# Optimization experiments

Hardware: AMD Instinct MI355X
Metric: run time of the kernel (lower is better)

## Reference

```python
import jax, jax.numpy as jnp
import numpy as np

ENT_N = 100000  # entity vocab (relation rows live inside this table, as in the source)
REL_N = 237
DIM = 128
N = 16384       # batch of triples
EPS = 1e-12     # F.normalize default eps


def _l2norm(x, axis=-1):
    n = jnp.linalg.norm(x, axis=axis, keepdims=True)
    return x / jnp.maximum(n, EPS)


def setup_inputs() -> dict:
    key = jax.random.key(0)
    k1, k2, k3, k4 = jax.random.split(key, 4)
    ent_emb = jax.random.normal(k1, (ENT_N, DIM), dtype=jnp.float32)
    h_ids = jax.random.randint(k2, (N,), 0, ENT_N)
    r_typ = jax.random.randint(k3, (N,), 0, REL_N)
    t_ids = jax.random.randint(k4, (N,), 0, ENT_N)
    return {"ent_emb": ent_emb, "h_ids": h_ids, "r_typ": r_typ, "t_ids": t_ids}


def reference(ent_emb, h_ids, r_typ, t_ids):
    d = ent_emb.shape[1]
    h = _l2norm(ent_emb[h_ids])           # [n, d]
    t = _l2norm(ent_emb[t_ids])           # [n, d]
    # The torch loop looks up ent_emb[r_typ*d + k] for k in range(d); gather
    # the whole relation block at once instead of d tiny lookups + cat.
    r_idx = r_typ[:, None] * d + jnp.arange(d)  # [n, d]
    R = ent_emb[r_idx]                     # [n, d, d]; row k = relation vec k
    prod = jnp.einsum('nd,nkd->nk', h, R)  # [n, d]
    prod = _l2norm(prod)
    return jnp.linalg.norm(prod - t, axis=1)  # [n]
```

## Files before the change

kernel.cpp:

```cpp
#include <hip/hip_runtime.h>

#define RELS 237
#define DIM 128
#define CH 32
#define MAXCHUNK 742
#define PREPB 64
#define EPS 1e-12f

typedef __attribute__((ext_vector_type(8))) short bf16x8;
typedef __attribute__((ext_vector_type(4))) float f32x4;


__device__ __forceinline__ unsigned short f2bf(float f) {
    unsigned int u = __float_as_uint(f);
    u = (u + 0x7fffu + ((u >> 16) & 1u)) >> 16;
    return (unsigned short)u;
}

__global__ __launch_bounds__(256) void k_prep(const int* __restrict__ r_typ,
                                              int* __restrict__ ws, int n) {
    __shared__ int hist[256];
    __shared__ int offs[256];
    __shared__ int scn[256];
    const int t = threadIdx.x;
    hist[t] = 0;
    __syncthreads();

    for (int i = blockIdx.x * 256 + t; i < n; i += PREPB * 256)
        atomicAdd(&hist[r_typ[i]], 1);
    __syncthreads();
    if (t < RELS && hist[t] > 0) atomicAdd(&ws[t], hist[t]);

    __syncthreads();
    __threadfence();
    if (t == 0) {
        atomicAdd(&ws[254], 1);
        while (atomicAdd(&ws[254], 0) < PREPB) __builtin_amdgcn_s_sleep(2);
    }
    __syncthreads();
    __threadfence();

    const int c = (t < RELS) ? atomicAdd(&ws[t], 0) : 0;
    scn[t] = c; __syncthreads();
    #pragma unroll
    for (int off = 1; off < 256; off <<= 1) {
        int v = (t >= off) ? scn[t - off] : 0;
        __syncthreads();
        scn[t] += v; __syncthreads();
    }
    offs[t] = scn[t] - c;
    __syncthreads();

    if (blockIdx.x == 0) {
        const int nch = (c + CH - 1) >> 5;
        scn[t] = nch; __syncthreads();
        #pragma unroll
        for (int off = 1; off < 256; off <<= 1) {
            int v = (t >= off) ? scn[t - off] : 0;
            __syncthreads();
            scn[t] += v; __syncthreads();
        }
        const int choff = scn[t] - nch;
        if (t == 255) ws[1000] = scn[255];
        for (int j = 0; j < nch; ++j) {
            int cb  = offs[t] + j * CH;
            int len = c - j * CH; if (len > CH) len = CH;
            ws[1024 + choff + j] = (t << 20) | (cb << 6) | len;
        }
    }

    for (int i = blockIdx.x * 256 + t; i < n; i += PREPB * 256) {
        int rr  = r_typ[i];
        int pos = offs[rr] + atomicAdd(&ws[512 + rr], 1);
        ws[2048 + pos] = i;
    }
}

__global__ __launch_bounds__(256, 3) void relgemm(
    const float* __restrict__ ent,
    const int*   __restrict__ h_ids,
    const int*   __restrict__ t_ids,
    const int*   __restrict__ ws,
    float*       __restrict__ out)
{
    __shared__ char smem[43648];
    unsigned short* Rb = (unsigned short*)smem;
    unsigned short* Hb = (unsigned short*)(smem + 34816);
    int*  sidx = (int*)(smem + 43520);
    float* Pp  = (float*)smem;

    const int cid = blockIdx.x;
    if (cid >= ws[1000]) return;
    const int e    = ws[1024 + cid];
    const int r    = e >> 20;
    const int base = (e >> 6) & 16383;
    const int len  = e & 63;
    const int* sorted = ws + 2048;

    const int tid  = threadIdx.x;
    const int lane = tid & 63;
    const int w    = tid >> 6;

    if (tid < CH) {
        int tc = tid < len ? tid : len - 1;
        sidx[tid] = sorted[base + tc];
    }
    __syncthreads();

    const float4* Rg = (const float4*)ent + ((long)r << 12);
    #pragma unroll
    for (int s = 0; s < 16; ++s) {
        int g = s * 256 + tid;
        int row = g >> 5, c4 = g & 31;
        float4 v = Rg[g];
        ushort4 b; b.x = f2bf(v.x); b.y = f2bf(v.y); b.z = f2bf(v.z); b.w = f2bf(v.w);
        *(ushort4*)(Rb + row * 136 + c4 * 4) = b;
    }
    #pragma unroll
    for (int s = 0; s < 4; ++s) {
        int g = s * 256 + tid;
        int trow = g >> 5, c4 = g & 31;
        int hid = h_ids[sidx[trow]];
        float4 v = ((const float4*)ent)[((long)hid << 5) + c4];
        ushort4 b; b.x = f2bf(v.x); b.y = f2bf(v.y); b.z = f2bf(v.z); b.w = f2bf(v.w);
        *(ushort4*)(Hb + trow * 136 + c4 * 4) = b;
    }
    __syncthreads();

    const int q = lane >> 4, c = lane & 15;
    const unsigned short* A0p = Hb + c * 136 + q * 8;
    const unsigned short* A1p = Hb + (c + 16) * 136 + q * 8;
    const unsigned short* B0p = Rb + (w * 32 + c) * 136 + q * 8;
    const unsigned short* B1p = Rb + (w * 32 + 16 + c) * 136 + q * 8;

    f32x4 a00 = {0.f,0.f,0.f,0.f}, a01 = a00, a10 = a00, a11 = a00;
    #pragma unroll
    for (int ks = 0; ks < 4; ++ks) {
        bf16x8 A0 = *(const bf16x8*)(A0p + ks * 32);
        bf16x8 A1 = *(const bf16x8*)(A1p + ks * 32);
        bf16x8 B0 = *(const bf16x8*)(B0p + ks * 32);
        bf16x8 B1 = *(const bf16x8*)(B1p + ks * 32);
        a00 = __builtin_amdgcn_mfma_f32_16x16x32_bf16(A0, B0, a00, 0, 0, 0);
        a01 = __builtin_amdgcn_mfma_f32_16x16x32_bf16(A0, B1, a01, 0, 0, 0);
        a10 = __builtin_amdgcn_mfma_f32_16x16x32_bf16(A1, B0, a10, 0, 0, 0);
        a11 = __builtin_amdgcn_mfma_f32_16x16x32_bf16(A1, B1, a11, 0, 0, 0);
    }
    __syncthreads();

    #pragma unroll
    for (int reg = 0; reg < 4; ++reg) {
        int m0 = q * 4 + reg;
        Pp[m0 * 132        + w * 32      + c] = a00[reg];
        Pp[m0 * 132        + w * 32 + 16 + c] = a01[reg];
        Pp[(m0 + 16) * 132 + w * 32      + c] = a10[reg];
        Pp[(m0 + 16) * 132 + w * 32 + 16 + c] = a11[reg];
    }
    __syncthreads();

    #pragma unroll
    for (int tt = 0; tt < 8; ++tt) {
        int t   = w * 8 + tt;
        int idx = sidx[t];
        int trow = __builtin_amdgcn_readfirstlane(t_ids[idx]);
        const float* tv = ent + ((long)trow << 7);
        float tv0 = tv[lane], tv1 = tv[lane + 64];
        float p0 = Pp[t * 132 + lane], p1 = Pp[t * 132 + 64 + lane];
        float sp  = p0 * p0 + p1 * p1;
        float st  = tv0 * tv0 + tv1 * tv1;
        float spt = p0 * tv0 + p1 * tv1;
        #pragma unroll
        for (int m = 32; m >= 1; m >>= 1) {
            sp  += __shfl_xor(sp,  m, 64);
            st  += __shfl_xor(st,  m, 64);
            spt += __shfl_xor(spt, m, 64);
        }
        if (lane == 0 && t < len) {
            float npn = fmaxf(sqrtf(sp), EPS);
            float ntn = fmaxf(sqrtf(st), EPS);
            float v   = 2.0f - 2.0f * (spt / (npn * ntn));
            out[idx] = sqrtf(fmaxf(v, 0.0f));
        }
    }
}

extern "C" void kernel_launch(void* const* d_in, const int* in_sizes, int n_in,
                              void* d_out, int out_size, void* d_ws, size_t ws_size,
                              hipStream_t stream) {
    const float* ent   = (const float*)d_in[0];
    const int*   h_ids = (const int*)d_in[1];
    const int*   r_typ = (const int*)d_in[2];
    const int*   t_ids = (const int*)d_in[3];
    float* out = (float*)d_out;
    int*   ws  = (int*)d_ws;
    const int n = in_sizes[1];

    hipMemsetAsync(ws, 0, 4096, stream);
    hipLaunchKernelGGL(k_prep,  dim3(PREPB),    dim3(256), 0, stream, r_typ, ws, n);
    hipLaunchKernelGGL(relgemm, dim3(MAXCHUNK), dim3(256), 0, stream,
                       ent, h_ids, t_ids, ws, out);
}
```

Before: 122.2 us.

## Pre-permute head/tail ids in prep and batch tail loads in epilogue

The prep kernel now scatters h_ids and t_ids into sorted order alongside the triple indices, so the GEMM kernel reads them contiguously instead of through a double indirection. The head-row gather is moved ahead of the relation-block load and no longer waits behind a barrier on sidx. The epilogue prefetches all eight tail rows and partial products into registers before the reductions, so their memory latency overlaps. In exchange, prep does extra global writes and the GEMM kernel uses more registers and a little more shared memory.

```diff
diff --git a/kernel.cpp b/kernel.cpp
--- a/kernel.cpp
+++ b/kernel.cpp
@@ -18,6 +18,8 @@
 }
 
 __global__ __launch_bounds__(256) void k_prep(const int* __restrict__ r_typ,
+                                              const int* __restrict__ h_ids,
+                                              const int* __restrict__ t_ids,
                                               int* __restrict__ ws, int n) {
     __shared__ int hist[256];
     __shared__ int offs[256];
@@ -71,22 +73,25 @@
 
     for (int i = blockIdx.x * 256 + t; i < n; i += PREPB * 256) {
         int rr  = r_typ[i];
+        int hi  = h_ids[i];
+        int ti  = t_ids[i];
         int pos = offs[rr] + atomicAdd(&ws[512 + rr], 1);
-        ws[2048 + pos] = i;
+        ws[2048  + pos] = i;
+        ws[18432 + pos] = hi;
+        ws[34816 + pos] = ti;
     }
 }
 
 __global__ __launch_bounds__(256, 3) void relgemm(
     const float* __restrict__ ent,
-    const int*   __restrict__ h_ids,
-    const int*   __restrict__ t_ids,
     const int*   __restrict__ ws,
     float*       __restrict__ out)
 {
-    __shared__ char smem[43648];
+    __shared__ char smem[43776];
     unsigned short* Rb = (unsigned short*)smem;
     unsigned short* Hb = (unsigned short*)(smem + 34816);
     int*  sidx = (int*)(smem + 43520);
+    int*  tRow = (int*)(smem + 43648);
     float* Pp  = (float*)smem;
 
     const int cid = blockIdx.x;
@@ -95,7 +100,9 @@
     const int r    = e >> 20;
     const int base = (e >> 6) & 16383;
     const int len  = e & 63;
-    const int* sorted = ws + 2048;
+    const int* sortedIdx = ws + 2048;
+    const int* shid      = ws + 18432;
+    const int* stid      = ws + 34816;
 
     const int tid  = threadIdx.x;
     const int lane = tid & 63;
@@ -103,10 +110,20 @@
 
     if (tid < CH) {
         int tc = tid < len ? tid : len - 1;
-        sidx[tid] = sorted[base + tc];
-    }
-    __syncthreads();
-
+        sidx[tid] = sortedIdx[base + tc];
+        tRow[tid] = stid[base + tc];
+    }
+
+    #pragma unroll
+    for (int s = 0; s < 4; ++s) {
+        int g = s * 256 + tid;
+        int trow = g >> 5, c4 = g & 31;
+        int tc = trow < len ? trow : len - 1;
+        int hid = shid[base + tc];
+        float4 v = ((const float4*)ent)[((long)hid << 5) + c4];
+        ushort4 b; b.x = f2bf(v.x); b.y = f2bf(v.y); b.z = f2bf(v.z); b.w = f2bf(v.w);
+        *(ushort4*)(Hb + trow * 136 + c4 * 4) = b;
+    }
     const float4* Rg = (const float4*)ent + ((long)r << 12);
     #pragma unroll
     for (int s = 0; s < 16; ++s) {
@@ -115,15 +132,6 @@
         float4 v = Rg[g];
         ushort4 b; b.x = f2bf(v.x); b.y = f2bf(v.y); b.z = f2bf(v.z); b.w = f2bf(v.w);
         *(ushort4*)(Rb + row * 136 + c4 * 4) = b;
-    }
-    #pragma unroll
-    for (int s = 0; s < 4; ++s) {
-        int g = s * 256 + tid;
-        int trow = g >> 5, c4 = g & 31;
-        int hid = h_ids[sidx[trow]];
-        float4 v = ((const float4*)ent)[((long)hid << 5) + c4];
-        ushort4 b; b.x = f2bf(v.x); b.y = f2bf(v.y); b.z = f2bf(v.z); b.w = f2bf(v.w);
-        *(ushort4*)(Hb + trow * 136 + c4 * 4) = b;
     }
     __syncthreads();
 
@@ -157,14 +165,22 @@
     }
     __syncthreads();
 
+    float p0v[8], p1v[8], t0v[8], t1v[8];
+    #pragma unroll
+    for (int tt = 0; tt < 8; ++tt) {
+        int t = w * 8 + tt;
+        int trow = tRow[t];
+        const float* tv = ent + ((long)trow << 7);
+        t0v[tt] = tv[lane];
+        t1v[tt] = tv[lane + 64];
+        p0v[tt] = Pp[t * 132 + lane];
+        p1v[tt] = Pp[t * 132 + 64 + lane];
+    }
     #pragma unroll
     for (int tt = 0; tt < 8; ++tt) {
         int t   = w * 8 + tt;
-        int idx = sidx[t];
-        int trow = __builtin_amdgcn_readfirstlane(t_ids[idx]);
-        const float* tv = ent + ((long)trow << 7);
-        float tv0 = tv[lane], tv1 = tv[lane + 64];
-        float p0 = Pp[t * 132 + lane], p1 = Pp[t * 132 + 64 + lane];
+        float p0 = p0v[tt], p1 = p1v[tt];
+        float tv0 = t0v[tt], tv1 = t1v[tt];
         float sp  = p0 * p0 + p1 * p1;
         float st  = tv0 * tv0 + tv1 * tv1;
         float spt = p0 * tv0 + p1 * tv1;
@@ -178,7 +194,7 @@
             float npn = fmaxf(sqrtf(sp), EPS);
             float ntn = fmaxf(sqrtf(st), EPS);
             float v   = 2.0f - 2.0f * (spt / (npn * ntn));
-            out[idx] = sqrtf(fmaxf(v, 0.0f));
+            out[sidx[t]] = sqrtf(fmaxf(v, 0.0f));
         }
     }
 }
@@ -195,7 +211,8 @@
     const int n = in_sizes[1];
 
     hipMemsetAsync(ws, 0, 4096, stream);
-    hipLaunchKernelGGL(k_prep,  dim3(PREPB),    dim3(256), 0, stream, r_typ, ws, n);
+    hipLaunchKernelGGL(k_prep,  dim3(PREPB),    dim3(256), 0, stream,
+                       r_typ, h_ids, t_ids, ws, n);
     hipLaunchKernelGGL(relgemm, dim3(MAXCHUNK), dim3(256), 0, stream,
-                       ent, h_ids, t_ids, ws, out);
-}
+                       ent, ws, out);
+}
```

After: 119.3 us. 2.4% less time.
